# Performance work log

Measured on AMD Instinct MI355X. Metric: run time of the kernel, lower is better.

The kernel has to match this reference:

```python
import jax, jax.numpy as jnp
import numpy as np

N_Q = 10000
B, S = 128, 200
M = 50          # memory_size
DK = 64         # memory_key_state_dim == q_embed_dim == final_fc_dim
DV = 128        # memory_value_state_dim == qa_embed_dim
F = 64          # final_fc_dim


def setup_inputs() -> dict:
    key = jax.random.key(0)
    ks = jax.random.split(key, 14)
    q_data = jax.random.randint(ks[0], (B, S), 0, N_Q + 1)
    qa_data = jax.random.randint(ks[1], (B, S), 0, 2 * N_Q + 1)
    # target in {-1 (pad), 0, 1}
    target = jax.random.randint(ks[2], (B, S), -1, 2).astype(jnp.float32)
    q_embed_w = jax.random.normal(ks[3], (N_Q + 1, DK), jnp.float32) * 0.1
    q_embed_w = q_embed_w.at[0].set(0.0)  # padding_idx=0
    qa_embed_w = jax.random.normal(ks[4], (2 * N_Q + 1, DV), jnp.float32) * 0.1
    qa_embed_w = qa_embed_w.at[0].set(0.0)
    mem_key = jax.random.normal(ks[5], (M, DK), jnp.float32) * (2.0 / DK) ** 0.5
    init_mem_value = jax.random.normal(ks[6], (M, DV), jnp.float32) * (2.0 / DV) ** 0.5
    erase_w = jax.random.normal(ks[7], (DV, DV), jnp.float32) * (2.0 / DV) ** 0.5
    erase_b = jnp.zeros((DV,), jnp.float32)
    add_w = jax.random.normal(ks[8], (DV, DV), jnp.float32) * (2.0 / DV) ** 0.5
    add_b = jnp.zeros((DV,), jnp.float32)
    read_w = jax.random.normal(ks[9], (F, DV + F), jnp.float32) * (2.0 / (DV + F)) ** 0.5
    read_b = jnp.zeros((F,), jnp.float32)
    pred_w = jax.random.normal(ks[10], (1, F), jnp.float32) * (2.0 / F) ** 0.5
    pred_b = jnp.zeros((1,), jnp.float32)
    return {
        'q_data': q_data, 'qa_data': qa_data, 'target': target,
        'q_embed_w': q_embed_w, 'qa_embed_w': qa_embed_w,
        'mem_key': mem_key, 'init_mem_value': init_mem_value,
        'erase_w': erase_w, 'erase_b': erase_b,
        'add_w': add_w, 'add_b': add_b,
        'read_w': read_w, 'read_b': read_b,
        'pred_w': pred_w, 'pred_b': pred_b,
    }


def reference(q_data, qa_data, target, q_embed_w, qa_embed_w, mem_key,
              init_mem_value, erase_w, erase_b, add_w, add_b,
              read_w, read_b, pred_w, pred_b):
    q_e = q_embed_w[q_data]    # [B,S,DK]
    qa_e = qa_embed_w[qa_data]  # [B,S,DV]
    Mv0 = jnp.broadcast_to(init_mem_value, (q_data.shape[0],) + init_mem_value.shape)  # [B,M,DV]

    def step(Mv, x):
        q, qa = x                                           # [B,DK], [B,DV]
        w = jax.nn.softmax(q @ mem_key.T, axis=1)           # addressing -> [B,M]
        read = jnp.einsum('bm,bmv->bv', w, Mv)              # weighted read (before write)
        e = jax.nn.sigmoid(qa @ erase_w.T + erase_b)        # [B,DV]
        a = jnp.tanh(qa @ add_w.T + add_b)                  # [B,DV]
        Mv_new = Mv * (1.0 - w[:, :, None] * e[:, None, :]) + w[:, :, None] * a[:, None, :]
        return Mv_new, read

    _, reads = jax.lax.scan(step, Mv0, (q_e.transpose(1, 0, 2), qa_e.transpose(1, 0, 2)))
    reads = reads.transpose(1, 0, 2)                        # [B,S,DV]

    h = jnp.tanh(jnp.concatenate([reads, q_e], axis=-1) @ read_w.T + read_b)  # [B,S,F]
    logits = (h @ pred_w.T + pred_b)[..., 0]                # [B,S]

    mask = target >= 0
    t = jnp.where(mask, target, 0.0)
    # stable BCE with logits
    bce = jnp.maximum(logits, 0.0) - logits * t + jnp.log1p(jnp.exp(-jnp.abs(logits)))
    n_valid = jnp.maximum(jnp.sum(mask.astype(jnp.float32)), 1.0)
    loss = jnp.sum(jnp.where(mask, bce, 0.0)) / n_valid
    probs = jnp.where(mask, jax.nn.sigmoid(logits), 0.0)    # masked predictions, fixed shape
    return loss, probs
```

## Files before the change

kernel.cpp:

```cpp
#include <hip/hip_runtime.h>
#include <math.h>

#define BB 128
#define SS 200
#define MM 50
#define DKK 64
#define DVV 128
#define FF 64
#define NROW (BB*SS)

#define WROW 64
#define NFCB (NROW/64)
#define WLDS 136
#define FLDS 200
#define CLEN 25
#define MPH 13
#define NSCB 100

#define W_OFF   0L
#define EA_OFF  (W_OFF + (long)NROW*WROW)
#define R_OFF   (EA_OFF + (long)NROW*DVV*2)
#define ACC_OFF (R_OFF + (long)NROW*DVV)

typedef __attribute__((ext_vector_type(8))) short bf16x8;
typedef __attribute__((ext_vector_type(4))) float f32x4;
typedef __attribute__((ext_vector_type(2))) float f32x2;

__device__ __forceinline__ short f2bf(float f) {
    unsigned u = __builtin_bit_cast(unsigned, f);
    u += 0x7fff + ((u >> 16) & 1);
    return (short)(u >> 16);
}
__device__ __forceinline__ bf16x8 cvt8(const float* p) {
    float4 lo = *(const float4*)p;
    float4 hi = *(const float4*)(p + 4);
    bf16x8 f;
    f[0] = f2bf(lo.x); f[1] = f2bf(lo.y); f[2] = f2bf(lo.z); f[3] = f2bf(lo.w);
    f[4] = f2bf(hi.x); f[5] = f2bf(hi.y); f[6] = f2bf(hi.z); f[7] = f2bf(hi.w);
    return f;
}

__global__ __launch_bounds__(256) void k_pre(const int* __restrict__ q_data,
                                             const float* __restrict__ q_embed_w,
                                             const float* __restrict__ mem_key,
                                             const int* __restrict__ qa_data,
                                             const float* __restrict__ qa_embed_w,
                                             const float* __restrict__ erase_w,
                                             const float* __restrict__ erase_b,
                                             const float* __restrict__ add_w,
                                             const float* __restrict__ add_b,
                                             float* __restrict__ w_out,
                                             float* __restrict__ EA,
                                             float* __restrict__ acc) {
    __shared__ union {
        short  wl[2 * 128 * WLDS];
        float4 mk[MM * 16];
    } sh;
    int tid = threadIdx.x;
    int bid = blockIdx.x;

    if (bid < NSCB) {
        if (bid == 0 && tid == 0) {
            acc[0] = 0.f; acc[1] = 0.f;
            ((unsigned*)acc)[2] = 0u;
        }
        const float4* mkg = (const float4*)mem_key;
        for (int i = tid; i < MM * 16; i += 256) sh.mk[i] = mkg[i];
        __syncthreads();

        int item = bid * 256 + tid;
        int qidx = q_data[item];
        const float4* qg = (const float4*)(q_embed_w + (long)qidx * DKK);
        float4 q[16];
#pragma unroll
        for (int i = 0; i < 16; i++) q[i] = qg[i];

        float s[MM];
        float mx = -1e30f;
#pragma unroll 2
        for (int m = 0; m < MM; m++) {
            float a = 0.f;
#pragma unroll
            for (int k4 = 0; k4 < 16; k4++) {
                float4 mkv = sh.mk[m * 16 + k4];
                float4 qv = q[k4];
                a = fmaf(qv.x, mkv.x, a);
                a = fmaf(qv.y, mkv.y, a);
                a = fmaf(qv.z, mkv.z, a);
                a = fmaf(qv.w, mkv.w, a);
            }
            s[m] = a;
            mx = fmaxf(mx, a);
        }
        float sum = 0.f;
#pragma unroll
        for (int m = 0; m < MM; m++) { s[m] = expf(s[m] - mx); sum += s[m]; }
        float inv = 1.f / sum;

        float* wo = w_out + (long)item * WROW;
#pragma unroll
        for (int m = 0; m < MM; m++) wo[m] = s[m] * inv;
#pragma unroll
        for (int m = MM; m < WROW; m++) wo[m] = 0.f;
        return;
    }

    int r0 = (bid - NSCB) * 64;
    int lane = tid & 63;
    int wv = tid >> 6;
    int n = lane & 15;
    int quad = lane >> 4;

    for (int i = tid; i < 8192; i += 256) {
        int mat = i >> 12;
        int r = (i >> 5) & 127;
        int p = i & 31;
        float4 src = *(const float4*)((mat ? add_w : erase_w) + r * 128 + p * 4);
        short4 d;
        d.x = f2bf(src.x); d.y = f2bf(src.y); d.z = f2bf(src.z); d.w = f2bf(src.w);
        *(short4*)(sh.wl + (mat * 128 + r) * WLDS + p * 4) = d;
    }

    int arow = r0 + wv * 16 + n;
    int qidx = qa_data[arow];
    const float* qp = qa_embed_w + (long)qidx * DVV + quad * 8;
    bf16x8 afrag[4];
#pragma unroll
    for (int kb = 0; kb < 4; kb++) afrag[kb] = cvt8(qp + kb * 32);

    float eb_[8], ab_[8];
#pragma unroll
    for (int vt = 0; vt < 8; vt++) {
        eb_[vt] = erase_b[vt * 16 + n];
        ab_[vt] = add_b[vt * 16 + n];
    }
    __syncthreads();

    int rowbase = r0 + wv * 16 + quad * 4;
#pragma unroll 2
    for (int vt = 0; vt < 8; vt++) {
        int vrow = vt * 16 + n;
        f32x4 ae = {0.f, 0.f, 0.f, 0.f};
        f32x4 aa = {0.f, 0.f, 0.f, 0.f};
#pragma unroll
        for (int kb = 0; kb < 4; kb++) {
            bf16x8 be = *(const bf16x8*)(sh.wl + vrow * WLDS + kb * 32 + quad * 8);
            bf16x8 ba = *(const bf16x8*)(sh.wl + (128 + vrow) * WLDS + kb * 32 + quad * 8);
            ae = __builtin_amdgcn_mfma_f32_16x16x32_bf16(afrag[kb], be, ae, 0, 0, 0);
            aa = __builtin_amdgcn_mfma_f32_16x16x32_bf16(afrag[kb], ba, aa, 0, 0, 0);
        }
        int v = vt * 16 + n;
        float eb = eb_[vt], ab = ab_[vt];
#pragma unroll
        for (int r = 0; r < 4; r++) {
            float ev = 1.f / (1.f + __expf(-(ae[r] + eb)));
            float av = 2.f / (1.f + __expf(-2.f * (aa[r] + ab))) - 1.f;
            float2 o; o.x = ev; o.y = av;
            *(float2*)(EA + (((long)(rowbase + r)) * DVV + v) * 2) = o;
        }
    }
}

__device__ __forceinline__ void scan_pass1(const float2* __restrict__ wp, int j0,
                                           const float* __restrict__ eab,
                                           f32x2* A2, f32x2* B2) {
    const f32x2 one = {1.f, 1.f};
    float2 e0 = *(const float2*)eab;
    float2 e1 = *(const float2*)(eab + (long)1 * DVV * 2);
#pragma unroll 1
    for (int t = 0; t < CLEN; t++) {
        int tp = (t + 2 < CLEN) ? t + 2 : CLEN - 1;
        float2 en = *(const float2*)(eab + (long)tp * DVV * 2);
        f32x2 ne2 = {-e0.x, -e0.x};
        f32x2 a2  = {e0.y, e0.y};
#pragma unroll
        for (int j = 0; j < MPH; j++) {
            float2 q = wp[t * 32 + j0 + j];
            f32x2 w2 = {q.x, q.y};
            f32x2 al = w2 * ne2 + one;
            A2[j] = A2[j] * al;
            B2[j] = al * B2[j] + w2 * a2;
        }
        e0 = e1; e1 = en;
    }
}

__device__ __forceinline__ void scan_pass2(const float2* __restrict__ wp, int j0,
                                           const float* __restrict__ eab,
                                           float* __restrict__ Rb, int mh,
                                           f32x2* Mv) {
    float2 e0 = *(const float2*)eab;
    float2 e1 = *(const float2*)(eab + (long)1 * DVV * 2);
#pragma unroll 1
    for (int t = 0; t < CLEN; t++) {
        int tp = (t + 2 < CLEN) ? t + 2 : CLEN - 1;
        float2 en = *(const float2*)(eab + (long)tp * DVV * 2);
        f32x2 ne2 = {-e0.x, -e0.x};
        f32x2 a2  = {e0.y, e0.y};
        f32x2 rd  = {0.f, 0.f};
#pragma unroll
        for (int j = 0; j < MPH; j++) {
            float2 q = wp[t * 32 + j0 + j];
            f32x2 w2 = {q.x, q.y};
            rd = rd + w2 * Mv[j];
            f32x2 s = ne2 * Mv[j] + a2;
            Mv[j] = Mv[j] + w2 * s;
        }
        float r = rd.x + rd.y;
        r += __shfl_xor(r, 32, 64);
        if (mh == 0) Rb[t * DVV] = r;
        e0 = e1; e1 = en;
    }
}

__global__ __launch_bounds__(512, 2) void k_scan(const float* __restrict__ w_pad,
                                                 const float* __restrict__ EA,
                                                 const float* __restrict__ init_mv,
                                                 float* __restrict__ R) {
    __shared__ float Wl[SS * WROW];
    __shared__ float Sb[52 * 32];
    int b   = blockIdx.x >> 2;
    int vq  = blockIdx.x & 3;
    int tid = threadIdx.x;
    int lane  = tid & 63;
    int chunk = tid >> 6;
    int mh = lane >> 5;
    int vl = lane & 31;
    int v  = vq * 32 + vl;
    int j0 = mh * MPH;
    int t0 = chunk * CLEN;

    {
        const float4* wg = (const float4*)(w_pad + (long)b * SS * WROW);
        float4* wl4 = (float4*)Wl;
        for (int i = tid; i < SS * WROW / 4; i += 512) wl4[i] = wg[i];
    }
    __syncthreads();

    const float2* wp  = (const float2*)(Wl + t0 * WROW);
    const float*  eab = EA + (((long)b * SS + t0) * DVV + v) * 2;
    float*        Rb  = R + ((long)b * SS + t0) * DVV + v;

    const f32x2 one = {1.f, 1.f};
    f32x2 A2[MPH], B2[MPH];
    f32x2 Mv[MPH];

    if (chunk == 0) {
#pragma unroll
        for (int j = 0; j < MPH; j++) {
            int m0 = 2 * (j0 + j), m1 = m0 + 1;
            if (m0 > MM - 2) m0 = MM - 2;
            if (m1 > MM - 1) m1 = MM - 1;
            Mv[j].x = init_mv[m0 * DVV + v];
            Mv[j].y = init_mv[m1 * DVV + v];
        }
        scan_pass2(wp, j0, eab, Rb, mh, Mv);
#pragma unroll
        for (int j = 0; j < MPH; j++) {
            Sb[(2 * (j0 + j)) * 32 + vl] = Mv[j].x;
            Sb[(2 * (j0 + j) + 1) * 32 + vl] = Mv[j].y;
        }
    } else if (chunk < 7) {
#pragma unroll
        for (int j = 0; j < MPH; j++) { A2[j] = one; B2[j] = (f32x2){0.f, 0.f}; }
        scan_pass1(wp, j0, eab, A2, B2);
    }
    __syncthreads();

    for (int c = 1; c < 8; c++) {
        if (chunk == c) {
#pragma unroll
            for (int j = 0; j < MPH; j++) {
                Mv[j].x = Sb[(2 * (j0 + j)) * 32 + vl];
                Mv[j].y = Sb[(2 * (j0 + j) + 1) * 32 + vl];
            }
            if (c < 7) {
#pragma unroll
                for (int j = 0; j < MPH; j++) {
                    f32x2 nb = A2[j] * Mv[j] + B2[j];
                    Sb[(2 * (j0 + j)) * 32 + vl] = nb.x;
                    Sb[(2 * (j0 + j) + 1) * 32 + vl] = nb.y;
                }
            }
        }
        __syncthreads();
    }

    if (chunk > 0) scan_pass2(wp, j0, eab, Rb, mh, Mv);
}

__global__ __launch_bounds__(256) void k_fc(const float* __restrict__ Rr,
                                            const int* __restrict__ q_data,
                                            const float* __restrict__ q_embed_w,
                                            const float* __restrict__ read_w,
                                            const float* __restrict__ read_b,
                                            const float* __restrict__ pred_w,
                                            const float* __restrict__ pred_b,
                                            const float* __restrict__ target,
                                            float* __restrict__ out,
                                            float* __restrict__ acc) {
    __shared__ short Wl[64 * FLDS];
    __shared__ float2 red[4];
    int tid = threadIdx.x;
    int r0 = blockIdx.x * 64;
    int lane = tid & 63;
    int wv = tid >> 6;
    int n = lane & 15;
    int quad = lane >> 4;

    for (int i = tid; i < 3072; i += 256) {
        int f = i / 48, p = i - f * 48;
        float4 src = *(const float4*)(read_w + f * 192 + p * 4);
        short4 d;
        d.x = f2bf(src.x); d.y = f2bf(src.y); d.z = f2bf(src.z); d.w = f2bf(src.w);
        *(short4*)(Wl + f * FLDS + p * 4) = d;
    }

    int arow = r0 + wv * 16 + n;
    const float* rp = Rr + (long)arow * DVV + quad * 8;
    int qi = q_data[arow];
    const float* qp = q_embed_w + (long)qi * DKK + quad * 8;
    bf16x8 afrag[6];
#pragma unroll
    for (int kb = 0; kb < 4; kb++) afrag[kb] = cvt8(rp + kb * 32);
#pragma unroll
    for (int kb = 0; kb < 2; kb++) afrag[4 + kb] = cvt8(qp + kb * 32);

    float rb_[4], pw_[4];
#pragma unroll
    for (int ft = 0; ft < 4; ft++) {
        rb_[ft] = read_b[ft * 16 + n];
        pw_[ft] = pred_w[ft * 16 + n];
    }
    float pb = pred_b[0];
    __syncthreads();

    int rowbase = r0 + wv * 16 + quad * 4;
    float pv[4] = {0.f, 0.f, 0.f, 0.f};
#pragma unroll
    for (int ft = 0; ft < 4; ft++) {
        int f = ft * 16 + n;
        f32x4 ac = {0.f, 0.f, 0.f, 0.f};
#pragma unroll
        for (int kb = 0; kb < 6; kb++) {
            bf16x8 bfr = *(const bf16x8*)(Wl + f * FLDS + kb * 32 + quad * 8);
            ac = __builtin_amdgcn_mfma_f32_16x16x32_bf16(afrag[kb], bfr, ac, 0, 0, 0);
        }
        float rb = rb_[ft], pw = pw_[ft];
#pragma unroll
        for (int r = 0; r < 4; r++) {
            float h = 2.f / (1.f + __expf(-2.f * (ac[r] + rb))) - 1.f;
            pv[r] = fmaf(pw, h, pv[r]);
        }
    }

    float bce_sum = 0.f, cnt = 0.f;
#pragma unroll
    for (int r = 0; r < 4; r++) {
        float p = pv[r];
        p += __shfl_xor(p, 1, 64);
        p += __shfl_xor(p, 2, 64);
        p += __shfl_xor(p, 4, 64);
        p += __shfl_xor(p, 8, 64);
        if (n == 0) {
            int row = rowbase + r;
            float tgt = target[row];
            float logit = p + pb;
            float prob = 0.f;
            if (tgt >= 0.f) {
                prob = 1.f / (1.f + __expf(-logit));
                float bce = fmaxf(logit, 0.f) - logit * tgt + log1pf(__expf(-fabsf(logit)));
                bce_sum += bce;
                cnt += 1.f;
            }
            out[1 + row] = prob;
        }
    }
    bce_sum += __shfl_xor(bce_sum, 16, 64);
    bce_sum += __shfl_xor(bce_sum, 32, 64);
    cnt     += __shfl_xor(cnt, 16, 64);
    cnt     += __shfl_xor(cnt, 32, 64);
    if (lane == 0) { red[wv].x = bce_sum; red[wv].y = cnt; }
    __syncthreads();
    if (tid == 0) {
        float bsum = red[0].x + red[1].x + red[2].x + red[3].x;
        float csum = red[0].y + red[1].y + red[2].y + red[3].y;
        atomicAdd(&acc[0], bsum);
        atomicAdd(&acc[1], csum);
        __threadfence();
        unsigned prev = atomicAdd((unsigned*)acc + 2, 1u);
        if (prev == NFCB - 1) {
            __threadfence();
            float B = atomicAdd(&acc[0], 0.f);
            float C = atomicAdd(&acc[1], 0.f);
            out[0] = B / fmaxf(C, 1.f);
        }
    }
}

extern "C" void kernel_launch(void* const* d_in, const int* in_sizes, int n_in,
                              void* d_out, int out_size, void* d_ws, size_t ws_size,
                              hipStream_t stream) {
    const int*   q_data     = (const int*)d_in[0];
    const int*   qa_data    = (const int*)d_in[1];
    const float* target     = (const float*)d_in[2];
    const float* q_embed_w  = (const float*)d_in[3];
    const float* qa_embed_w = (const float*)d_in[4];
    const float* mem_key    = (const float*)d_in[5];
    const float* init_mv    = (const float*)d_in[6];
    const float* erase_w    = (const float*)d_in[7];
    const float* erase_b    = (const float*)d_in[8];
    const float* add_w      = (const float*)d_in[9];
    const float* add_b      = (const float*)d_in[10];
    const float* read_w     = (const float*)d_in[11];
    const float* read_b     = (const float*)d_in[12];
    const float* pred_w     = (const float*)d_in[13];
    const float* pred_b     = (const float*)d_in[14];
    float* out = (float*)d_out;
    float* ws  = (float*)d_ws;

    float* w_all = ws + W_OFF;
    float* EA    = ws + EA_OFF;
    float* R     = ws + R_OFF;
    float* acc   = ws + ACC_OFF;

    k_pre<<<NSCB + NROW / 64, 256, 0, stream>>>(q_data, q_embed_w, mem_key,
                                                qa_data, qa_embed_w,
                                                erase_w, erase_b, add_w, add_b,
                                                w_all, EA, acc);
    k_scan<<<BB * 4, 512, 0, stream>>>(w_all, EA, init_mv, R);
    k_fc<<<NFCB, 256, 0, stream>>>(R, q_data, q_embed_w, read_w, read_b,
                                   pred_w, pred_b, target, out, acc);
}
```

Baseline: 174.5 us.

## Split scan across more time chunks and memory quarters per block

Reworks the chunked linear-recurrence scan. Each block now covers 16 value columns instead of 32, the memory dimension is split four ways per lane group instead of two, and time is cut into 16 chunks instead of 8, giving 1024-thread blocks and twice as many blocks. This shortens each thread's serial chain and register footprint. In exchange it adds a longer serial carry-propagation loop with 16 barriers, an extra shuffle reduction per step, and each block reloads the full per-batch W tile into LDS, doubling that traffic.

```diff
diff --git a/kernel.cpp b/kernel.cpp
--- a/kernel.cpp
+++ b/kernel.cpp
@@ -13,8 +13,8 @@
 #define NFCB (NROW/64)
 #define WLDS 136
 #define FLDS 200
-#define CLEN 25
-#define MPH 13
+#define NCH 16
+#define MPQ 7
 #define NSCB 100
 
 #define W_OFF   0L
@@ -161,20 +161,20 @@
     }
 }
 
-__device__ __forceinline__ void scan_pass1(const float2* __restrict__ wp, int j0,
+__device__ __forceinline__ void scan_pass1(const float2* __restrict__ wp, int j0, int L,
                                            const float* __restrict__ eab,
                                            f32x2* A2, f32x2* B2) {
     const f32x2 one = {1.f, 1.f};
     float2 e0 = *(const float2*)eab;
     float2 e1 = *(const float2*)(eab + (long)1 * DVV * 2);
 #pragma unroll 1
-    for (int t = 0; t < CLEN; t++) {
-        int tp = (t + 2 < CLEN) ? t + 2 : CLEN - 1;
+    for (int t = 0; t < L; t++) {
+        int tp = (t + 2 < L) ? t + 2 : L - 1;
         float2 en = *(const float2*)(eab + (long)tp * DVV * 2);
         f32x2 ne2 = {-e0.x, -e0.x};
         f32x2 a2  = {e0.y, e0.y};
 #pragma unroll
-        for (int j = 0; j < MPH; j++) {
+        for (int j = 0; j < MPQ; j++) {
             float2 q = wp[t * 32 + j0 + j];
             f32x2 w2 = {q.x, q.y};
             f32x2 al = w2 * ne2 + one;
@@ -185,21 +185,21 @@
     }
 }
 
-__device__ __forceinline__ void scan_pass2(const float2* __restrict__ wp, int j0,
+__device__ __forceinline__ void scan_pass2(const float2* __restrict__ wp, int j0, int L,
                                            const float* __restrict__ eab,
-                                           float* __restrict__ Rb, int mh,
+                                           float* __restrict__ Rb, int quad,
                                            f32x2* Mv) {
     float2 e0 = *(const float2*)eab;
     float2 e1 = *(const float2*)(eab + (long)1 * DVV * 2);
 #pragma unroll 1
-    for (int t = 0; t < CLEN; t++) {
-        int tp = (t + 2 < CLEN) ? t + 2 : CLEN - 1;
+    for (int t = 0; t < L; t++) {
+        int tp = (t + 2 < L) ? t + 2 : L - 1;
         float2 en = *(const float2*)(eab + (long)tp * DVV * 2);
         f32x2 ne2 = {-e0.x, -e0.x};
         f32x2 a2  = {e0.y, e0.y};
         f32x2 rd  = {0.f, 0.f};
 #pragma unroll
-        for (int j = 0; j < MPH; j++) {
+        for (int j = 0; j < MPQ; j++) {
             float2 q = wp[t * 32 + j0 + j];
             f32x2 w2 = {q.x, q.y};
             rd = rd + w2 * Mv[j];
@@ -207,33 +207,35 @@
             Mv[j] = Mv[j] + w2 * s;
         }
         float r = rd.x + rd.y;
+        r += __shfl_xor(r, 16, 64);
         r += __shfl_xor(r, 32, 64);
-        if (mh == 0) Rb[t * DVV] = r;
+        if (quad == 0) Rb[t * DVV] = r;
         e0 = e1; e1 = en;
     }
 }
 
-__global__ __launch_bounds__(512, 2) void k_scan(const float* __restrict__ w_pad,
-                                                 const float* __restrict__ EA,
-                                                 const float* __restrict__ init_mv,
-                                                 float* __restrict__ R) {
+__global__ __launch_bounds__(1024, 1) void k_scan(const float* __restrict__ w_pad,
+                                                  const float* __restrict__ EA,
+                                                  const float* __restrict__ init_mv,
+                                                  float* __restrict__ R) {
     __shared__ float Wl[SS * WROW];
-    __shared__ float Sb[52 * 32];
-    int b   = blockIdx.x >> 2;
-    int vq  = blockIdx.x & 3;
+    __shared__ float Sb[56 * 16];
+    int b   = blockIdx.x >> 3;
+    int vg  = blockIdx.x & 7;
     int tid = threadIdx.x;
     int lane  = tid & 63;
     int chunk = tid >> 6;
-    int mh = lane >> 5;
-    int vl = lane & 31;
-    int v  = vq * 32 + vl;
-    int j0 = mh * MPH;
-    int t0 = chunk * CLEN;
+    int quad = lane >> 4;
+    int vl = lane & 15;
+    int v  = vg * 16 + vl;
+    int j0 = quad * MPQ;
+    int t0 = (chunk < 8) ? chunk * 13 : 104 + (chunk - 8) * 12;
+    int L  = (chunk < 8) ? 13 : 12;
 
     {
         const float4* wg = (const float4*)(w_pad + (long)b * SS * WROW);
         float4* wl4 = (float4*)Wl;
-        for (int i = tid; i < SS * WROW / 4; i += 512) wl4[i] = wg[i];
+        for (int i = tid; i < SS * WROW / 4; i += 1024) wl4[i] = wg[i];
     }
     __syncthreads();
 
@@ -242,51 +244,51 @@
     float*        Rb  = R + ((long)b * SS + t0) * DVV + v;
 
     const f32x2 one = {1.f, 1.f};
-    f32x2 A2[MPH], B2[MPH];
-    f32x2 Mv[MPH];
+    f32x2 A2[MPQ], B2[MPQ];
+    f32x2 Mv[MPQ];
 
     if (chunk == 0) {
 #pragma unroll
-        for (int j = 0; j < MPH; j++) {
+        for (int j = 0; j < MPQ; j++) {
             int m0 = 2 * (j0 + j), m1 = m0 + 1;
             if (m0 > MM - 2) m0 = MM - 2;
             if (m1 > MM - 1) m1 = MM - 1;
             Mv[j].x = init_mv[m0 * DVV + v];
             Mv[j].y = init_mv[m1 * DVV + v];
         }
-        scan_pass2(wp, j0, eab, Rb, mh, Mv);
-#pragma unroll
-        for (int j = 0; j < MPH; j++) {
-            Sb[(2 * (j0 + j)) * 32 + vl] = Mv[j].x;
-            Sb[(2 * (j0 + j) + 1) * 32 + vl] = Mv[j].y;
-        }
-    } else if (chunk < 7) {
-#pragma unroll
-        for (int j = 0; j < MPH; j++) { A2[j] = one; B2[j] = (f32x2){0.f, 0.f}; }
-        scan_pass1(wp, j0, eab, A2, B2);
+        scan_pass2(wp, j0, L, eab, Rb, quad, Mv);
+#pragma unroll
+        for (int j = 0; j < MPQ; j++) {
+            Sb[(2 * (j0 + j)) * 16 + vl] = Mv[j].x;
+            Sb[(2 * (j0 + j) + 1) * 16 + vl] = Mv[j].y;
+        }
+    } else if (chunk < NCH - 1) {
+#pragma unroll
+        for (int j = 0; j < MPQ; j++) { A2[j] = one; B2[j] = (f32x2){0.f, 0.f}; }
+        scan_pass1(wp, j0, L, eab, A2, B2);
     }
     __syncthreads();
 
-    for (int c = 1; c < 8; c++) {
+    for (int c = 1; c < NCH; c++) {
         if (chunk == c) {
 #pragma unroll
-            for (int j = 0; j < MPH; j++) {
-                Mv[j].x = Sb[(2 * (j0 + j)) * 32 + vl];
-                Mv[j].y = Sb[(2 * (j0 + j) + 1) * 32 + vl];
+            for (int j = 0; j < MPQ; j++) {
+                Mv[j].x = Sb[(2 * (j0 + j)) * 16 + vl];
+                Mv[j].y = Sb[(2 * (j0 + j) + 1) * 16 + vl];
             }
-            if (c < 7) {
-#pragma unroll
-                for (int j = 0; j < MPH; j++) {
+            if (c < NCH - 1) {
+#pragma unroll
+                for (int j = 0; j < MPQ; j++) {
                     f32x2 nb = A2[j] * Mv[j] + B2[j];
-                    Sb[(2 * (j0 + j)) * 32 + vl] = nb.x;
-                    Sb[(2 * (j0 + j) + 1) * 32 + vl] = nb.y;
+                    Sb[(2 * (j0 + j)) * 16 + vl] = nb.x;
+                    Sb[(2 * (j0 + j) + 1) * 16 + vl] = nb.y;
                 }
             }
         }
         __syncthreads();
     }
 
-    if (chunk > 0) scan_pass2(wp, j0, eab, Rb, mh, Mv);
+    if (chunk > 0) scan_pass2(wp, j0, L, eab, Rb, quad, Mv);
 }
 
 __global__ __launch_bounds__(256) void k_fc(const float* __restrict__ Rr,
@@ -428,7 +430,7 @@
                                                 qa_data, qa_embed_w,
                                                 erase_w, erase_b, add_w, add_b,
                                                 w_all, EA, acc);
-    k_scan<<<BB * 4, 512, 0, stream>>>(w_all, EA, init_mv, R);
+    k_scan<<<BB * 8, 1024, 0, stream>>>(w_all, EA, init_mv, R);
     k_fc<<<NFCB, 256, 0, stream>>>(R, q_data, q_embed_w, read_w, read_b,
                                    pred_w, pred_b, target, out, acc);
 }
```

Result: slower. 187.8 us (+7.6%).
